# Optimization experiments

Measured on AMD Instinct MI355X. Metric: run time of the kernel, lower is better.

The kernel has to match this reference:

```python
import jax, jax.numpy as jnp
import numpy as np

EPS = 1e-5
NEG_SLOPE = 0.1  # GeoTransformer UnaryBlock uses LeakyReLU(0.1)
GROUPS = 32


def linear(x, W, b):
    # torch nn.Linear convention: W is (out, in)
    return x @ W.T + b


def group_norm(x, gamma, beta, groups=GROUPS):
    # x: (N, C). Torch applies GroupNorm on (1, C, N): stats over (C//g * N) per group.
    N, C = x.shape
    xg = x.T.reshape(groups, -1)            # (g, C//g * N)
    m = xg.mean(axis=1, keepdims=True)
    v = xg.var(axis=1, keepdims=True)
    xn = ((xg - m) / jnp.sqrt(v + EPS)).reshape(C, N).T
    return xn * gamma + beta


def unary_block(x, W, b, gamma, beta):
    return jax.nn.leaky_relu(group_norm(linear(x, W, b), gamma, beta), NEG_SLOPE)


def setup_inputs() -> dict:
    key = jax.random.key(0)
    ks = jax.random.split(key, 24)
    init_dim = 64
    N2, N3, N4, N5 = 131072, 32768, 8192, 2048
    d2, d3, d4, d5 = init_dim * 4, init_dim * 8, init_dim * 16, 2048
    out_dim = 256
    s = lambda k, shp: jax.random.normal(k, shp, dtype=jnp.float32)
    inp = {
        'feats_s2': s(ks[0], (N2, d2)),
        'feats_s3': s(ks[1], (N3, d3)),
        'feats_s4': s(ks[2], (N4, d4)),
        'feats_s5': s(ks[3], (N5, d5)),
        'up1': jax.random.randint(ks[4], (N2,), 0, N3),
        'up2': jax.random.randint(ks[5], (N3,), 0, N4),
        'up3': jax.random.randint(ks[6], (N4,), 0, N5),
        # inproj: Linear(input_dim, init_dim*32)
        'W_in': s(ks[7], (init_dim * 32, d5)) * 0.02,
        'b_in': s(ks[8], (init_dim * 32,)) * 0.02,
        # decoder4: UnaryBlock(init_dim*48, init_dim*16)
        'W4': s(ks[9], (init_dim * 16, init_dim * 48)) * 0.02,
        'b4': s(ks[10], (init_dim * 16,)) * 0.02,
        'g4': jnp.ones((init_dim * 16,), jnp.float32),
        'beta4': jnp.zeros((init_dim * 16,), jnp.float32),
        # decoder3: UnaryBlock(init_dim*24, init_dim*8)
        'W3': s(ks[11], (init_dim * 8, init_dim * 24)) * 0.02,
        'b3': s(ks[12], (init_dim * 8,)) * 0.02,
        'g3': jnp.ones((init_dim * 8,), jnp.float32),
        'beta3': jnp.zeros((init_dim * 8,), jnp.float32),
        # decoder2: LastUnaryBlock(init_dim*12, output_dim) -> plain Linear
        'W2': s(ks[13], (out_dim, init_dim * 12)) * 0.02,
        'b2': s(ks[14], (out_dim,)) * 0.02,
    }
    return inp


def reference(feats_s2, feats_s3, feats_s4, feats_s5, up1, up2, up3,
              W_in, b_in, W4, b4, g4, beta4, W3, b3, g3, beta3, W2, b2):
    x5 = linear(feats_s5, W_in, b_in)                     # (N5, 2048)
    l4 = jnp.concatenate([x5[up3], feats_s4], axis=1)     # gather + concat (N4, 3072)
    l4 = unary_block(l4, W4, b4, g4, beta4)               # (N4, 1024)
    l3 = jnp.concatenate([l4[up2], feats_s3], axis=1)     # (N3, 1536)
    l3 = unary_block(l3, W3, b3, g3, beta3)               # (N3, 512)
    l2 = jnp.concatenate([l3[up1], feats_s2], axis=1)     # (N2, 768)
    return linear(l2, W2, b2)                             # (N2, 256)
```

## Files before the change

kernel.cpp:

```cpp
#include <hip/hip_runtime.h>
#include <cstdint>
#include <cstddef>

#define DEVI __device__ __forceinline__
#define WAITVM0 asm volatile("s_waitcnt vmcnt(0)" ::: "memory")
#define WAITVM4 asm volatile("s_waitcnt vmcnt(4)" ::: "memory")
#define WAITVM8 asm volatile("s_waitcnt vmcnt(8)" ::: "memory")
#define WAITLGKM asm volatile("s_waitcnt lgkmcnt(0)" ::: "memory")
#define SCHEDB __builtin_amdgcn_sched_barrier(0)

typedef __bf16 bf16x8 __attribute__((ext_vector_type(8)));
typedef float f32x4 __attribute__((ext_vector_type(4)));
typedef uint32_t u32x4 __attribute__((ext_vector_type(4)));

DEVI ushort f2bf(float f) {
  union { float f; uint32_t u; } v; v.f = f;
  uint32_t u = v.u;
  return (ushort)((u + 0x7FFFu + ((u >> 16) & 1u)) >> 16);
}
DEVI float bf2f(ushort h) {
  union { uint32_t u; float f; } v; v.u = ((uint32_t)h) << 16;
  return v.f;
}
DEVI float lrelu(float t) { return t > 0.0f ? t : 0.1f * t; }

DEVI u32x4 cvt8(f32x4 a, f32x4 b) {
  u32x4 o;
  o[0] = (uint32_t)f2bf(a[0]) | ((uint32_t)f2bf(a[1]) << 16);
  o[1] = (uint32_t)f2bf(a[2]) | ((uint32_t)f2bf(a[3]) << 16);
  o[2] = (uint32_t)f2bf(b[0]) | ((uint32_t)f2bf(b[1]) << 16);
  o[3] = (uint32_t)f2bf(b[2]) | ((uint32_t)f2bf(b[3]) << 16);
  return o;
}
DEVI u32x4 gn8(u32x4 d, f32x4 g0, f32x4 g1, f32x4 b0, f32x4 b1) {
  float f0 = bf2f((ushort)(d[0] & 0xffffu)), f1 = bf2f((ushort)(d[0] >> 16));
  float f2 = bf2f((ushort)(d[1] & 0xffffu)), f3 = bf2f((ushort)(d[1] >> 16));
  float f4 = bf2f((ushort)(d[2] & 0xffffu)), f5 = bf2f((ushort)(d[2] >> 16));
  float f6 = bf2f((ushort)(d[3] & 0xffffu)), f7 = bf2f((ushort)(d[3] >> 16));
  float t0 = lrelu(f0 * g0[0] + b0[0]), t1 = lrelu(f1 * g0[1] + b0[1]);
  float t2 = lrelu(f2 * g0[2] + b0[2]), t3 = lrelu(f3 * g0[3] + b0[3]);
  float t4 = lrelu(f4 * g1[0] + b1[0]), t5 = lrelu(f5 * g1[1] + b1[1]);
  float t6 = lrelu(f6 * g1[2] + b1[2]), t7 = lrelu(f7 * g1[3] + b1[3]);
  u32x4 o;
  o[0] = (uint32_t)f2bf(t0) | ((uint32_t)f2bf(t1) << 16);
  o[1] = (uint32_t)f2bf(t2) | ((uint32_t)f2bf(t3) << 16);
  o[2] = (uint32_t)f2bf(t4) | ((uint32_t)f2bf(t5) << 16);
  o[3] = (uint32_t)f2bf(t6) | ((uint32_t)f2bf(t7) << 16);
  return o;
}

DEVI void async_copy16(const void* g, void* l) {
  __attribute__((address_space(1))) void* gp =
      reinterpret_cast<__attribute__((address_space(1))) void*>(
          reinterpret_cast<uintptr_t>(const_cast<void*>(g)));
  __attribute__((address_space(3))) void* lp =
      reinterpret_cast<__attribute__((address_space(3))) void*>(
          static_cast<uint32_t>(reinterpret_cast<uintptr_t>(l)));
  __builtin_amdgcn_global_load_lds(gp, lp, 16, 0, 0);
}

struct CvtSeg { const f32x4* src; u32x4* dst; };
struct CvtArgs { CvtSeg seg[4]; int start[5]; };

__global__ void cvt_multi(CvtArgs a, int total8) {
  int i = blockIdx.x * blockDim.x + threadIdx.x;
  const int stride = gridDim.x * blockDim.x;
  for (; i < total8; i += stride) {
    int s = 0;
#pragma unroll
    for (int j = 1; j < 4; ++j) s += (i >= a.start[j]);
    const int off = i - a.start[s];
    f32x4 f0 = a.seg[s].src[off * 2];
    f32x4 f1 = a.seg[s].src[off * 2 + 1];
    a.seg[s].dst[off] = cvt8(f0, f1);
  }
}

__global__ void zero_kernel(float* __restrict__ p) { p[threadIdx.x] = 0.0f; }

__global__ void gn_coef(const float* __restrict__ stats, const float* __restrict__ gamma,
                        const float* __restrict__ beta, float* __restrict__ ga,
                        float* __restrict__ be, int C, float invcnt) {
  int ch = blockIdx.x * blockDim.x + threadIdx.x;
  if (ch >= C) return;
  int g = ch / (C >> 5);
  float mean = stats[2 * g] * invcnt;
  float var = stats[2 * g + 1] * invcnt - mean * mean;
  float inv = rsqrtf(var + 1e-5f);
  float gm = gamma[ch] * inv;
  ga[ch] = gm;
  be[ch] = beta[ch] - mean * gm;
}

__global__ void gn_apply(const ushort* __restrict__ x, const float* __restrict__ ga,
                         const float* __restrict__ be, ushort* __restrict__ y,
                         int Nrows, int C) {
  const int tpr = C >> 3;
  const int gtid = blockIdx.x * blockDim.x + threadIdx.x;
  const int c8 = (gtid % tpr) * 8;
  const f32x4 g0 = *(const f32x4*)(ga + c8), g1 = *(const f32x4*)(ga + c8 + 4);
  const f32x4 b0 = *(const f32x4*)(be + c8), b1 = *(const f32x4*)(be + c8 + 4);
  const int rstep = (gridDim.x * blockDim.x) / tpr;
  for (int r = gtid / tpr; r < Nrows; r += rstep) {
    u32x4 d = *(const u32x4*)(x + (size_t)r * C + c8);
    *(u32x4*)(y + (size_t)r * C + c8) = gn8(d, g0, g1, b0, b1);
  }
}

template <int EPI, int STATS>
__global__ __launch_bounds__(256, 3) void gemms(
    const ushort* __restrict__ Ag, const float* __restrict__ Adf,
    const int* __restrict__ up, int dg,
    const ushort* __restrict__ Bw, const float* __restrict__ bias,
    void* __restrict__ Cout, float* __restrict__ stats,
    int M, int N, int K) {
  constexpr int BM = 128, BN = 128, BK = 64;
  constexpr int ABY = BM * BK * 2;
  __shared__ __align__(16) char smem[ABY + BN * BK * 2];
  __shared__ int s_up[BM];
  __shared__ float ssum[32], ssq[32];

  const int nbn = N >> 7;
  const int cpx = (int)gridDim.x >> 3;
  const int bid = ((int)blockIdx.x & 7) * cpx + ((int)blockIdx.x >> 3);
  const int bm = bid / nbn, bn = bid % nbn;
  const int row0 = bm * BM, col0 = bn * BN;
  const int tid = threadIdx.x, lane = tid & 63, wave = tid >> 6;
  const int wm = wave >> 1, wn = wave & 1;
  const int dd = K - dg;
  const int ng = dg / BK;
  const int nt = K / BK;

  if (up != nullptr && tid < BM) s_up[tid] = up[row0 + tid];
  if constexpr (STATS) { if (tid < 32) { ssum[tid] = 0.f; ssq[tid] = 0.f; } }
  __syncthreads();

  int cs_[4];
  const ushort* pG[4]; const float* pD[4];
#pragma unroll
  for (int li = 0; li < 4; ++li) {
    const int chunk = li * 256 + tid;
    const int r = chunk >> 3;
    cs_[li] = ((chunk & 7) ^ (r & 7)) << 3;
    pG[li] = (ng > 0) ? (Ag + (size_t)s_up[r] * dg + cs_[li]) : nullptr;
    pD[li] = (ng < nt) ? (Adf + (size_t)(row0 + r) * dd + cs_[li]) : nullptr;
  }
  const ushort* pB[4];
#pragma unroll
  for (int li = 0; li < 4; ++li) {
    const int chunk = li * 256 + tid;
    const int rb = chunk >> 3;
    pB[li] = Bw + (size_t)(col0 + rb) * K + (((chunk & 7) ^ (rb & 7)) << 3);
  }

  f32x4 rdv[8];

  auto issueAg = [&](int t) {
#pragma unroll
    for (int li = 0; li < 4; ++li)
      async_copy16(pG[li] + t * BK, smem + li * 4096 + wave * 1024);
  };
  auto issueB = [&](int t) {
#pragma unroll
    for (int li = 0; li < 4; ++li)
      async_copy16(pB[li] + t * BK, smem + ABY + li * 4096 + wave * 1024);
  };
  auto issueRdv = [&](int t) {
    const int kd = t * BK - dg;
#pragma unroll
    for (int li = 0; li < 4; ++li) {
      rdv[2 * li]     = *(const f32x4*)(pD[li] + kd);
      rdv[2 * li + 1] = *(const f32x4*)(pD[li] + kd + 4);
    }
  };
  auto dsWrite = [&]() {
#pragma unroll
    for (int li = 0; li < 4; ++li)
      *(u32x4*)(smem + li * 4096 + tid * 16) = cvt8(rdv[2 * li], rdv[2 * li + 1]);
  };

  int offA[2][4], offB[2][4];
#pragma unroll
  for (int kk = 0; kk < 2; ++kk) {
    const int ch = kk * 4 + (lane >> 4);
#pragma unroll
    for (int m = 0; m < 4; ++m) {
      const int ra = wm * 64 + m * 16 + (lane & 15);
      offA[kk][m] = ra * 128 + ((ch ^ (ra & 7)) << 4);
    }
#pragma unroll
    for (int n = 0; n < 4; ++n) {
      const int rb = wn * 64 + n * 16 + (lane & 15);
      offB[kk][n] = ABY + rb * 128 + ((ch ^ (rb & 7)) << 4);
    }
  }

  if (ng == 0) issueRdv(0);

  f32x4 acc[4][4] = {};
  for (int t = 0; t < nt; ++t) {
    const bool curD = (t >= ng);
    const bool nxtDirect = (t + 1 < nt) && (t + 1 >= ng);
    if (!curD) issueAg(t);
    issueB(t);
    if (curD) {
      WAITVM4;
      SCHEDB;
      dsWrite();
    }
    if (nxtDirect) issueRdv(t + 1);
    if (nxtDirect) { WAITVM8; } else { WAITVM0; }
    WAITLGKM;
    SCHEDB;
    __builtin_amdgcn_s_barrier();
#pragma unroll
    for (int kk = 0; kk < 2; ++kk) {
      bf16x8 af[4], bv[4];
#pragma unroll
      for (int m = 0; m < 4; ++m) af[m] = *(const bf16x8*)(smem + offA[kk][m]);
#pragma unroll
      for (int n = 0; n < 4; ++n) bv[n] = *(const bf16x8*)(smem + offB[kk][n]);
      __builtin_amdgcn_s_setprio(1);
#pragma unroll
      for (int m = 0; m < 4; ++m)
#pragma unroll
        for (int n = 0; n < 4; ++n)
          acc[m][n] = __builtin_amdgcn_mfma_f32_16x16x32_bf16(af[m], bv[n], acc[m][n], 0, 0, 0);
      __builtin_amdgcn_s_setprio(0);
    }
    __builtin_amdgcn_s_barrier();
  }

  const int cr = (lane >> 4) << 2;
  const int cc = lane & 15;
  float sacc[4] = {0, 0, 0, 0}, qacc[4] = {0, 0, 0, 0};
#pragma unroll
  for (int n = 0; n < 4; ++n) {
    const int colg = col0 + wn * 64 + n * 16 + cc;
    const float bvv = bias[colg];
#pragma unroll
    for (int m = 0; m < 4; ++m) {
      const int rowg = row0 + wm * 64 + m * 16 + cr;
#pragma unroll
      for (int r2 = 0; r2 < 4; ++r2) {
        const float v = acc[m][n][r2] + bvv;
        if constexpr (STATS) { sacc[n] += v; qacc[n] += v * v; }
        if constexpr (EPI == 0)
          ((ushort*)Cout)[(size_t)(rowg + r2) * N + colg] = f2bf(v);
        else
          ((float*)Cout)[(size_t)(rowg + r2) * N + colg] = v;
      }
    }
  }
  if constexpr (STATS) {
    const int gsize = N >> 5;
#pragma unroll
    for (int n = 0; n < 4; ++n) {
      float s = sacc[n], q = qacc[n];
      s += __shfl_xor(s, 16); q += __shfl_xor(q, 16);
      s += __shfl_xor(s, 32); q += __shfl_xor(q, 32);
      if (lane < 16) {
        const int colg = col0 + wn * 64 + n * 16 + lane;
        const int g = colg / gsize;
        atomicAdd(&ssum[g], s);
        atomicAdd(&ssq[g], q);
      }
    }
    __syncthreads();
    if (tid < 32) {
      const int g0 = col0 / gsize, g1 = (col0 + BN) / gsize;
      if (tid >= g0 && tid < g1) {
        atomicAdd(&stats[2 * tid], ssum[tid]);
        atomicAdd(&stats[2 * tid + 1], ssq[tid]);
      }
    }
  }
}

template <int EPI, int STATS>
__global__ __launch_bounds__(512, 3) void gemmw(
    const ushort* __restrict__ Ag, const float* __restrict__ Adf,
    const int* __restrict__ up, int dg,
    const ushort* __restrict__ Bw, const float* __restrict__ bias,
    void* __restrict__ Cout, float* __restrict__ stats,
    int M, int N, int K) {
  constexpr int BM = 128, BN = 256, BK = 64;
  constexpr int ABY = BM * BK * 2;
  __shared__ __align__(16) char smem[ABY + BN * BK * 2];
  __shared__ int s_up[BM];
  __shared__ float ssum[32], ssq[32];

  const int nbn = N >> 8;
  const int cpx = (int)gridDim.x >> 3;
  const int bid = ((int)blockIdx.x & 7) * cpx + ((int)blockIdx.x >> 3);
  const int bm = bid / nbn, bn = bid % nbn;
  const int row0 = bm * BM, col0 = bn * BN;
  const int tid = threadIdx.x, lane = tid & 63, wave = tid >> 6;
  const int wm = wave >> 2, wn = wave & 3;
  const int dd = K - dg;
  const int ng = dg / BK;
  const int nt = K / BK;

  if (up != nullptr && tid < BM) s_up[tid] = up[row0 + tid];
  if constexpr (STATS) { if (tid < 32) { ssum[tid] = 0.f; ssq[tid] = 0.f; } }
  __syncthreads();

  int cs_[2];
  const ushort* pG[2]; const float* pD[2];
#pragma unroll
  for (int li = 0; li < 2; ++li) {
    const int chunk = li * 512 + tid;
    const int r = chunk >> 3;
    cs_[li] = ((chunk & 7) ^ (r & 7)) << 3;
    pG[li] = (ng > 0) ? (Ag + (size_t)s_up[r] * dg + cs_[li]) : nullptr;
    pD[li] = (ng < nt) ? (Adf + (size_t)(row0 + r) * dd + cs_[li]) : nullptr;
  }
  const ushort* pB[4];
#pragma unroll
  for (int li = 0; li < 4; ++li) {
    const int chunk = li * 512 + tid;
    const int rb = chunk >> 3;
    pB[li] = Bw + (size_t)(col0 + rb) * K + (((chunk & 7) ^ (rb & 7)) << 3);
  }

  f32x4 rdv[4];

  auto issueAg = [&](int t) {
#pragma unroll
    for (int li = 0; li < 2; ++li)
      async_copy16(pG[li] + t * BK, smem + li * 8192 + wave * 1024);
  };
  auto issueB = [&](int t) {
#pragma unroll
    for (int li = 0; li < 4; ++li)
      async_copy16(pB[li] + t * BK, smem + ABY + li * 8192 + wave * 1024);
  };
  auto issueRdv = [&](int t) {
    const int kd = t * BK - dg;
#pragma unroll
    for (int li = 0; li < 2; ++li) {
      rdv[2 * li]     = *(const f32x4*)(pD[li] + kd);
      rdv[2 * li + 1] = *(const f32x4*)(pD[li] + kd + 4);
    }
  };
  auto dsWrite = [&]() {
#pragma unroll
    for (int li = 0; li < 2; ++li)
      *(u32x4*)(smem + li * 8192 + tid * 16) = cvt8(rdv[2 * li], rdv[2 * li + 1]);
  };

  int offA[2][4], offB[2][4];
#pragma unroll
  for (int kk = 0; kk < 2; ++kk) {
    const int ch = kk * 4 + (lane >> 4);
#pragma unroll
    for (int m = 0; m < 4; ++m) {
      const int ra = wm * 64 + m * 16 + (lane & 15);
      offA[kk][m] = ra * 128 + ((ch ^ (ra & 7)) << 4);
    }
#pragma unroll
    for (int n = 0; n < 4; ++n) {
      const int rb = wn * 64 + n * 16 + (lane & 15);
      offB[kk][n] = ABY + rb * 128 + ((ch ^ (rb & 7)) << 4);
    }
  }

  if (ng == 0) issueRdv(0);

  f32x4 acc[4][4] = {};
  for (int t = 0; t < nt; ++t) {
    const bool curD = (t >= ng);
    const bool nxtD = (t + 1 < nt) && (t + 1 >= ng);
    if (!curD) issueAg(t);
    issueB(t);
    if (curD) {
      WAITVM4;
      SCHEDB;
      dsWrite();
    }
    if (nxtD) issueRdv(t + 1);
    if (nxtD) { WAITVM4; } else { WAITVM0; }
    WAITLGKM;
    SCHEDB;
    __builtin_amdgcn_s_barrier();
#pragma unroll
    for (int kk = 0; kk < 2; ++kk) {
      bf16x8 af[4], bv[4];
#pragma unroll
      for (int m = 0; m < 4; ++m) af[m] = *(const bf16x8*)(smem + offA[kk][m]);
#pragma unroll
      for (int n = 0; n < 4; ++n) bv[n] = *(const bf16x8*)(smem + offB[kk][n]);
      __builtin_amdgcn_s_setprio(1);
#pragma unroll
      for (int m = 0; m < 4; ++m)
#pragma unroll
        for (int n = 0; n < 4; ++n)
          acc[m][n] = __builtin_amdgcn_mfma_f32_16x16x32_bf16(af[m], bv[n], acc[m][n], 0, 0, 0);
      __builtin_amdgcn_s_setprio(0);
    }
    __builtin_amdgcn_s_barrier();
  }

  const int cr = (lane >> 4) << 2;
  const int cc = lane & 15;
  float sacc[4] = {0, 0, 0, 0}, qacc[4] = {0, 0, 0, 0};
#pragma unroll
  for (int n = 0; n < 4; ++n) {
    const int colg = col0 + wn * 64 + n * 16 + cc;
    const float bvv = bias[colg];
#pragma unroll
    for (int m = 0; m < 4; ++m) {
      const int rowg = row0 + wm * 64 + m * 16 + cr;
#pragma unroll
      for (int r2 = 0; r2 < 4; ++r2) {
        const float v = acc[m][n][r2] + bvv;
        if constexpr (STATS) { sacc[n] += v; qacc[n] += v * v; }
        if constexpr (EPI == 0)
          ((ushort*)Cout)[(size_t)(rowg + r2) * N + colg] = f2bf(v);
        else
          ((float*)Cout)[(size_t)(rowg + r2) * N + colg] = v;
      }
    }
  }
  if constexpr (STATS) {
    const int gsize = N >> 5;
#pragma unroll
    for (int n = 0; n < 4; ++n) {
      float s = sacc[n], q = qacc[n];
      s += __shfl_xor(s, 16); q += __shfl_xor(q, 16);
      s += __shfl_xor(s, 32); q += __shfl_xor(q, 32);
      if (lane < 16) {
        const int colg = col0 + wn * 64 + n * 16 + lane;
        const int g = colg / gsize;
        atomicAdd(&ssum[g], s);
        atomicAdd(&ssq[g], q);
      }
    }
    __syncthreads();
    if (tid < 32) {
      const int g0 = col0 / gsize, g1 = (col0 + BN) / gsize;
      if (tid >= g0 && tid < g1) {
        atomicAdd(&stats[2 * tid], ssum[tid]);
        atomicAdd(&stats[2 * tid + 1], ssq[tid]);
      }
    }
  }
}

extern "C" void kernel_launch(void* const* d_in, const int* in_sizes, int n_in,
                              void* d_out, int out_size, void* d_ws, size_t ws_size,
                              hipStream_t stream) {
  const float* s2   = (const float*)d_in[0];
  const float* s3   = (const float*)d_in[1];
  const float* s4   = (const float*)d_in[2];
  const float* s5   = (const float*)d_in[3];
  const int*   up1  = (const int*)d_in[4];
  const int*   up2  = (const int*)d_in[5];
  const int*   up3  = (const int*)d_in[6];
  const float* W_in = (const float*)d_in[7];
  const float* b_in = (const float*)d_in[8];
  const float* W4   = (const float*)d_in[9];
  const float* b4   = (const float*)d_in[10];
  const float* g4   = (const float*)d_in[11];
  const float* bt4  = (const float*)d_in[12];
  const float* W3   = (const float*)d_in[13];
  const float* b3   = (const float*)d_in[14];
  const float* g3   = (const float*)d_in[15];
  const float* bt3  = (const float*)d_in[16];
  const float* W2   = (const float*)d_in[17];
  const float* b2   = (const float*)d_in[18];
  float* out = (float*)d_out;
  char* ws = (char*)d_ws;

  ushort* Winb  = (ushort*)(ws + 0);
  ushort* W4b   = (ushort*)(ws + 8388608);
  ushort* W3b   = (ushort*)(ws + 14680064);
  ushort* W2b   = (ushort*)(ws + 16252928);
  float*  stats = (float*)(ws + 16646144);
  float*  cga4  = (float*)(ws + 16646656);
  float*  cbe4  = (float*)(ws + 16650752);
  float*  cga3  = (float*)(ws + 16654848);
  float*  cbe3  = (float*)(ws + 16656896);
  ushort* x5b   = (ushort*)(ws + 16777216);
  ushort* l4lin = (ushort*)(ws + 25165824);
  ushort* l4b   = (ushort*)(ws + 41943040);
  ushort* l3lin = (ushort*)(ws + 58720256);
  ushort* l3b   = (ushort*)(ws + 92274688);

  zero_kernel<<<1, 128, 0, stream>>>(stats);

  CvtArgs ca;
  const float* srcs[4] = { W_in, W4, W3, W2 };
  ushort* dsts[4] = { Winb, W4b, W3b, W2b };
  long ns[4] = { 2048L*2048, 1024L*3072, 512L*1536, 256L*768 };
  int cum = 0;
  for (int i = 0; i < 4; ++i) {
    ca.seg[i].src = (const f32x4*)srcs[i];
    ca.seg[i].dst = (u32x4*)dsts[i];
    ca.start[i] = cum;
    cum += (int)(ns[i] >> 3);
  }
  ca.start[4] = cum;
  cvt_multi<<<1024, 256, 0, stream>>>(ca, cum);

  gemms<0, 0><<<256, 256, 0, stream>>>(
      nullptr, s5, nullptr, 0, Winb, b_in, x5b, nullptr, 2048, 2048, 2048);
  gemmw<0, 1><<<256, 512, 0, stream>>>(
      x5b, s4, up3, 2048, W4b, b4, l4lin, stats, 8192, 1024, 3072);
  gn_coef<<<4, 256, 0, stream>>>(stats, g4, bt4, cga4, cbe4, 1024, 1.0f / 262144.0f);
  gn_apply<<<2048, 256, 0, stream>>>(l4lin, cga4, cbe4, l4b, 8192, 1024);
  gemmw<0, 1><<<512, 512, 0, stream>>>(
      l4b, s3, up2, 1024, W3b, b3, l3lin, stats + 64, 32768, 512, 1536);
  gn_coef<<<2, 256, 0, stream>>>(stats + 64, g3, bt3, cga3, cbe3, 512, 1.0f / 524288.0f);
  gn_apply<<<2048, 256, 0, stream>>>(l3lin, cga3, cbe3, l3b, 32768, 512);
  gemmw<1, 0><<<1024, 512, 0, stream>>>(
      l3b, s2, up1, 512, W2b, b2, out, nullptr, 131072, 256, 768);

  (void)in_sizes; (void)n_in; (void)out_size; (void)ws_size;
}
```

Before: 362.5 us.

## Fuse GroupNorm into decoder GEMMs via cooperative grid sync

Replaces the GEMM → gn_coef → gn_apply sequence for decoder4 and decoder3 with one cooperative kernel. Each block keeps its accumulators in registers, adds its group statistics atomically, waits on a grid-wide sync, then applies the normalisation and LeakyReLU before writing bf16 output. This removes the intermediate pre-norm write and re-read plus two launches per layer. In exchange it uses 128x128 tiles with 256 threads, needs SUB=2 row tiles held in registers for layer 3, and depends on all 512 blocks being co-resident. The final linear layer also moves from the wide kernel to the 128x128 kernel.

```diff
diff --git a/kernel.cpp b/kernel.cpp
--- a/kernel.cpp
+++ b/kernel.cpp
@@ -1,4 +1,5 @@
 #include <hip/hip_runtime.h>
+#include <hip/hip_cooperative_groups.h>
 #include <cstdint>
 #include <cstddef>
 
@@ -30,22 +31,6 @@
   o[1] = (uint32_t)f2bf(a[2]) | ((uint32_t)f2bf(a[3]) << 16);
   o[2] = (uint32_t)f2bf(b[0]) | ((uint32_t)f2bf(b[1]) << 16);
   o[3] = (uint32_t)f2bf(b[2]) | ((uint32_t)f2bf(b[3]) << 16);
-  return o;
-}
-DEVI u32x4 gn8(u32x4 d, f32x4 g0, f32x4 g1, f32x4 b0, f32x4 b1) {
-  float f0 = bf2f((ushort)(d[0] & 0xffffu)), f1 = bf2f((ushort)(d[0] >> 16));
-  float f2 = bf2f((ushort)(d[1] & 0xffffu)), f3 = bf2f((ushort)(d[1] >> 16));
-  float f4 = bf2f((ushort)(d[2] & 0xffffu)), f5 = bf2f((ushort)(d[2] >> 16));
-  float f6 = bf2f((ushort)(d[3] & 0xffffu)), f7 = bf2f((ushort)(d[3] >> 16));
-  float t0 = lrelu(f0 * g0[0] + b0[0]), t1 = lrelu(f1 * g0[1] + b0[1]);
-  float t2 = lrelu(f2 * g0[2] + b0[2]), t3 = lrelu(f3 * g0[3] + b0[3]);
-  float t4 = lrelu(f4 * g1[0] + b1[0]), t5 = lrelu(f5 * g1[1] + b1[1]);
-  float t6 = lrelu(f6 * g1[2] + b1[2]), t7 = lrelu(f7 * g1[3] + b1[3]);
-  u32x4 o;
-  o[0] = (uint32_t)f2bf(t0) | ((uint32_t)f2bf(t1) << 16);
-  o[1] = (uint32_t)f2bf(t2) | ((uint32_t)f2bf(t3) << 16);
-  o[2] = (uint32_t)f2bf(t4) | ((uint32_t)f2bf(t5) << 16);
-  o[3] = (uint32_t)f2bf(t6) | ((uint32_t)f2bf(t7) << 16);
   return o;
 }
 
@@ -77,35 +62,6 @@
 }
 
 __global__ void zero_kernel(float* __restrict__ p) { p[threadIdx.x] = 0.0f; }
-
-__global__ void gn_coef(const float* __restrict__ stats, const float* __restrict__ gamma,
-                        const float* __restrict__ beta, float* __restrict__ ga,
-                        float* __restrict__ be, int C, float invcnt) {
-  int ch = blockIdx.x * blockDim.x + threadIdx.x;
-  if (ch >= C) return;
-  int g = ch / (C >> 5);
-  float mean = stats[2 * g] * invcnt;
-  float var = stats[2 * g + 1] * invcnt - mean * mean;
-  float inv = rsqrtf(var + 1e-5f);
-  float gm = gamma[ch] * inv;
-  ga[ch] = gm;
-  be[ch] = beta[ch] - mean * gm;
-}
-
-__global__ void gn_apply(const ushort* __restrict__ x, const float* __restrict__ ga,
-                         const float* __restrict__ be, ushort* __restrict__ y,
-                         int Nrows, int C) {
-  const int tpr = C >> 3;
-  const int gtid = blockIdx.x * blockDim.x + threadIdx.x;
-  const int c8 = (gtid % tpr) * 8;
-  const f32x4 g0 = *(const f32x4*)(ga + c8), g1 = *(const f32x4*)(ga + c8 + 4);
-  const f32x4 b0 = *(const f32x4*)(be + c8), b1 = *(const f32x4*)(be + c8 + 4);
-  const int rstep = (gridDim.x * blockDim.x) / tpr;
-  for (int r = gtid / tpr; r < Nrows; r += rstep) {
-    u32x4 d = *(const u32x4*)(x + (size_t)r * C + c8);
-    *(u32x4*)(y + (size_t)r * C + c8) = gn8(d, g0, g1, b0, b1);
-  }
-}
 
 template <int EPI, int STATS>
 __global__ __launch_bounds__(256, 3) void gemms(
@@ -277,77 +233,42 @@
   }
 }
 
-template <int EPI, int STATS>
-__global__ __launch_bounds__(512, 3) void gemmw(
+template <int SUB>
+__global__ void gemmc(
     const ushort* __restrict__ Ag, const float* __restrict__ Adf,
     const int* __restrict__ up, int dg,
     const ushort* __restrict__ Bw, const float* __restrict__ bias,
-    void* __restrict__ Cout, float* __restrict__ stats,
-    int M, int N, int K) {
-  constexpr int BM = 128, BN = 256, BK = 64;
+    const float* __restrict__ gamma, const float* __restrict__ beta,
+    ushort* __restrict__ Cout, float* __restrict__ stats,
+    int M, int N, int K, float invcnt) {
+  constexpr int BM = 128, BN = 128, BK = 64;
   constexpr int ABY = BM * BK * 2;
   __shared__ __align__(16) char smem[ABY + BN * BK * 2];
   __shared__ int s_up[BM];
   __shared__ float ssum[32], ssq[32];
-
-  const int nbn = N >> 8;
+  __shared__ float sst[64];
+
+  const int nbn = N >> 7;
   const int cpx = (int)gridDim.x >> 3;
   const int bid = ((int)blockIdx.x & 7) * cpx + ((int)blockIdx.x >> 3);
-  const int bm = bid / nbn, bn = bid % nbn;
-  const int row0 = bm * BM, col0 = bn * BN;
+  const int bm0 = (bid / nbn) * SUB;
+  const int bn = bid % nbn;
+  const int col0 = bn * BN;
   const int tid = threadIdx.x, lane = tid & 63, wave = tid >> 6;
-  const int wm = wave >> 2, wn = wave & 3;
+  const int wm = wave >> 1, wn = wave & 1;
   const int dd = K - dg;
   const int ng = dg / BK;
   const int nt = K / BK;
 
-  if (up != nullptr && tid < BM) s_up[tid] = up[row0 + tid];
-  if constexpr (STATS) { if (tid < 32) { ssum[tid] = 0.f; ssq[tid] = 0.f; } }
-  __syncthreads();
-
-  int cs_[2];
-  const ushort* pG[2]; const float* pD[2];
-#pragma unroll
-  for (int li = 0; li < 2; ++li) {
-    const int chunk = li * 512 + tid;
-    const int r = chunk >> 3;
-    cs_[li] = ((chunk & 7) ^ (r & 7)) << 3;
-    pG[li] = (ng > 0) ? (Ag + (size_t)s_up[r] * dg + cs_[li]) : nullptr;
-    pD[li] = (ng < nt) ? (Adf + (size_t)(row0 + r) * dd + cs_[li]) : nullptr;
-  }
+  if (tid < 32) { ssum[tid] = 0.f; ssq[tid] = 0.f; }
+
   const ushort* pB[4];
 #pragma unroll
   for (int li = 0; li < 4; ++li) {
-    const int chunk = li * 512 + tid;
+    const int chunk = li * 256 + tid;
     const int rb = chunk >> 3;
     pB[li] = Bw + (size_t)(col0 + rb) * K + (((chunk & 7) ^ (rb & 7)) << 3);
   }
-
-  f32x4 rdv[4];
-
-  auto issueAg = [&](int t) {
-#pragma unroll
-    for (int li = 0; li < 2; ++li)
-      async_copy16(pG[li] + t * BK, smem + li * 8192 + wave * 1024);
-  };
-  auto issueB = [&](int t) {
-#pragma unroll
-    for (int li = 0; li < 4; ++li)
-      async_copy16(pB[li] + t * BK, smem + ABY + li * 8192 + wave * 1024);
-  };
-  auto issueRdv = [&](int t) {
-    const int kd = t * BK - dg;
-#pragma unroll
-    for (int li = 0; li < 2; ++li) {
-      rdv[2 * li]     = *(const f32x4*)(pD[li] + kd);
-      rdv[2 * li + 1] = *(const f32x4*)(pD[li] + kd + 4);
-    }
-  };
-  auto dsWrite = [&]() {
-#pragma unroll
-    for (int li = 0; li < 2; ++li)
-      *(u32x4*)(smem + li * 8192 + tid * 16) = cvt8(rdv[2 * li], rdv[2 * li + 1]);
-  };
 
   int offA[2][4], offB[2][4];
 #pragma unroll
@@ -365,83 +286,152 @@
     }
   }
 
-  if (ng == 0) issueRdv(0);
-
-  f32x4 acc[4][4] = {};
-  for (int t = 0; t < nt; ++t) {
-    const bool curD = (t >= ng);
-    const bool nxtD = (t + 1 < nt) && (t + 1 >= ng);
-    if (!curD) issueAg(t);
-    issueB(t);
-    if (curD) {
-      WAITVM4;
+  f32x4 acc[SUB][4][4] = {};
+
+#pragma unroll
+  for (int s = 0; s < SUB; ++s) {
+    const int row0 = (bm0 + s) * BM;
+    __syncthreads();
+    if (tid < BM) s_up[tid] = up[row0 + tid];
+    __syncthreads();
+
+    int cs_[4];
+    const ushort* pG[4]; const float* pD[4];
+#pragma unroll
+    for (int li = 0; li < 4; ++li) {
+      const int chunk = li * 256 + tid;
+      const int r = chunk >> 3;
+      cs_[li] = ((chunk & 7) ^ (r & 7)) << 3;
+      pG[li] = Ag + (size_t)s_up[r] * dg + cs_[li];
+      pD[li] = Adf + (size_t)(row0 + r) * dd + cs_[li];
+    }
+
+    f32x4 rdv[8];
+    auto issueAg = [&](int t) {
+#pragma unroll
+      for (int li = 0; li < 4; ++li)
+        async_copy16(pG[li] + t * BK, smem + li * 4096 + wave * 1024);
+    };
+    auto issueB = [&](int t) {
+#pragma unroll
+      for (int li = 0; li < 4; ++li)
+        async_copy16(pB[li] + t * BK, smem + ABY + li * 4096 + wave * 1024);
+    };
+    auto issueRdv = [&](int t) {
+      const int kd = t * BK - dg;
+#pragma unroll
+      for (int li = 0; li < 4; ++li) {
+        rdv[2 * li]     = *(const f32x4*)(pD[li] + kd);
+        rdv[2 * li + 1] = *(const f32x4*)(pD[li] + kd + 4);
+      }
+    };
+    auto dsWrite = [&]() {
+#pragma unroll
+      for (int li = 0; li < 4; ++li)
+        *(u32x4*)(smem + li * 4096 + tid * 16) = cvt8(rdv[2 * li], rdv[2 * li + 1]);
+    };
+
+    if (ng == 0) issueRdv(0);
+
+    for (int t = 0; t < nt; ++t) {
+      const bool curD = (t >= ng);
+      const bool nxtDirect = (t + 1 < nt) && (t + 1 >= ng);
+      if (!curD) issueAg(t);
+      issueB(t);
+      if (curD) {
+        WAITVM4;
+        SCHEDB;
+        dsWrite();
+      }
+      if (nxtDirect) issueRdv(t + 1);
+      if (nxtDirect) { WAITVM8; } else { WAITVM0; }
+      WAITLGKM;
       SCHEDB;
-      dsWrite();
-    }
-    if (nxtD) issueRdv(t + 1);
-    if (nxtD) { WAITVM4; } else { WAITVM0; }
-    WAITLGKM;
-    SCHEDB;
-    __builtin_amdgcn_s_barrier();
-#pragma unroll
-    for (int kk = 0; kk < 2; ++kk) {
-      bf16x8 af[4], bv[4];
-#pragma unroll
-      for (int m = 0; m < 4; ++m) af[m] = *(const bf16x8*)(smem + offA[kk][m]);
-#pragma unroll
-      for (int n = 0; n < 4; ++n) bv[n] = *(const bf16x8*)(smem + offB[kk][n]);
-      __builtin_amdgcn_s_setprio(1);
-#pragma unroll
-      for (int m = 0; m < 4; ++m)
-#pragma unroll
-        for (int n = 0; n < 4; ++n)
-          acc[m][n] = __builtin_amdgcn_mfma_f32_16x16x32_bf16(af[m], bv[n], acc[m][n], 0, 0, 0);
-      __builtin_amdgcn_s_setprio(0);
-    }
-    __builtin_amdgcn_s_barrier();
+      __builtin_amdgcn_s_barrier();
+#pragma unroll
+      for (int kk = 0; kk < 2; ++kk) {
+        bf16x8 af[4], bv[4];
+#pragma unroll
+        for (int m = 0; m < 4; ++m) af[m] = *(const bf16x8*)(smem + offA[kk][m]);
+#pragma unroll
+        for (int n = 0; n < 4; ++n) bv[n] = *(const bf16x8*)(smem + offB[kk][n]);
+        __builtin_amdgcn_s_setprio(1);
+#pragma unroll
+        for (int m = 0; m < 4; ++m)
+#pragma unroll
+          for (int n = 0; n < 4; ++n)
+            acc[s][m][n] = __builtin_amdgcn_mfma_f32_16x16x32_bf16(af[m], bv[n], acc[s][m][n], 0, 0, 0);
+        __builtin_amdgcn_s_setprio(0);
+      }
+      __builtin_amdgcn_s_barrier();
+    }
   }
 
   const int cr = (lane >> 4) << 2;
   const int cc = lane & 15;
+  const int gsize = N >> 5;
   float sacc[4] = {0, 0, 0, 0}, qacc[4] = {0, 0, 0, 0};
 #pragma unroll
   for (int n = 0; n < 4; ++n) {
     const int colg = col0 + wn * 64 + n * 16 + cc;
     const float bvv = bias[colg];
 #pragma unroll
-    for (int m = 0; m < 4; ++m) {
-      const int rowg = row0 + wm * 64 + m * 16 + cr;
-#pragma unroll
-      for (int r2 = 0; r2 < 4; ++r2) {
-        const float v = acc[m][n][r2] + bvv;
-        if constexpr (STATS) { sacc[n] += v; qacc[n] += v * v; }
-        if constexpr (EPI == 0)
-          ((ushort*)Cout)[(size_t)(rowg + r2) * N + colg] = f2bf(v);
-        else
-          ((float*)Cout)[(size_t)(rowg + r2) * N + colg] = v;
-      }
-    }
-  }
-  if constexpr (STATS) {
-    const int gsize = N >> 5;
-#pragma unroll
-    for (int n = 0; n < 4; ++n) {
-      float s = sacc[n], q = qacc[n];
-      s += __shfl_xor(s, 16); q += __shfl_xor(q, 16);
-      s += __shfl_xor(s, 32); q += __shfl_xor(q, 32);
-      if (lane < 16) {
-        const int colg = col0 + wn * 64 + n * 16 + lane;
-        const int g = colg / gsize;
-        atomicAdd(&ssum[g], s);
-        atomicAdd(&ssq[g], q);
-      }
-    }
-    __syncthreads();
-    if (tid < 32) {
-      const int g0 = col0 / gsize, g1 = (col0 + BN) / gsize;
-      if (tid >= g0 && tid < g1) {
-        atomicAdd(&stats[2 * tid], ssum[tid]);
-        atomicAdd(&stats[2 * tid + 1], ssq[tid]);
+    for (int s = 0; s < SUB; ++s)
+#pragma unroll
+      for (int m = 0; m < 4; ++m)
+#pragma unroll
+        for (int r2 = 0; r2 < 4; ++r2) {
+          const float v = acc[s][m][n][r2] + bvv;
+          sacc[n] += v; qacc[n] += v * v;
+        }
+  }
+#pragma unroll
+  for (int n = 0; n < 4; ++n) {
+    float s = sacc[n], q = qacc[n];
+    s += __shfl_xor(s, 16); q += __shfl_xor(q, 16);
+    s += __shfl_xor(s, 32); q += __shfl_xor(q, 32);
+    if (lane < 16) {
+      const int colg = col0 + wn * 64 + n * 16 + lane;
+      const int g = colg / gsize;
+      atomicAdd(&ssum[g], s);
+      atomicAdd(&ssq[g], q);
+    }
+  }
+  __syncthreads();
+  if (tid < 32) {
+    const int g0 = col0 / gsize, g1 = (col0 + BN) / gsize;
+    if (tid >= g0 && tid < g1) {
+      atomicAdd(&stats[2 * tid], ssum[tid]);
+      atomicAdd(&stats[2 * tid + 1], ssq[tid]);
+    }
+  }
+
+  cooperative_groups::this_grid().sync();
+
+  if (tid < 64) sst[tid] = atomicAdd(&stats[tid], 0.0f);
+  __syncthreads();
+
+#pragma unroll
+  for (int n = 0; n < 4; ++n) {
+    const int colg = col0 + wn * 64 + n * 16 + cc;
+    const int g = colg / gsize;
+    const float mean = sst[2 * g] * invcnt;
+    const float var  = sst[2 * g + 1] * invcnt - mean * mean;
+    const float inv  = rsqrtf(var + 1e-5f);
+    const float ga = gamma[colg] * inv;
+    const float be = beta[colg] - mean * ga;
+    const float bvv = bias[colg];
+#pragma unroll
+    for (int s = 0; s < SUB; ++s) {
+      const int row0 = (bm0 + s) * BM;
+#pragma unroll
+      for (int m = 0; m < 4; ++m) {
+        const int rowg = row0 + wm * 64 + m * 16 + cr;
+#pragma unroll
+        for (int r2 = 0; r2 < 4; ++r2) {
+          const float v = acc[s][m][n][r2] + bvv;
+          Cout[(size_t)(rowg + r2) * N + colg] = f2bf(lrelu(v * ga + be));
+        }
       }
     }
   }
@@ -477,15 +467,9 @@
   ushort* W3b   = (ushort*)(ws + 14680064);
   ushort* W2b   = (ushort*)(ws + 16252928);
   float*  stats = (float*)(ws + 16646144);
-  float*  cga4  = (float*)(ws + 16646656);
-  float*  cbe4  = (float*)(ws + 16650752);
-  float*  cga3  = (float*)(ws + 16654848);
-  float*  cbe3  = (float*)(ws + 16656896);
   ushort* x5b   = (ushort*)(ws + 16777216);
-  ushort* l4lin = (ushort*)(ws + 25165824);
-  ushort* l4b   = (ushort*)(ws + 41943040);
-  ushort* l3lin = (ushort*)(ws + 58720256);
-  ushort* l3b   = (ushort*)(ws + 92274688);
+  ushort* l4b   = (ushort*)(ws + 25165824);
+  ushort* l3b   = (ushort*)(ws + 41943040);
 
   zero_kernel<<<1, 128, 0, stream>>>(stats);
 
@@ -505,15 +489,26 @@
 
   gemms<0, 0><<<256, 256, 0, stream>>>(
       nullptr, s5, nullptr, 0, Winb, b_in, x5b, nullptr, 2048, 2048, 2048);
-  gemmw<0, 1><<<256, 512, 0, stream>>>(
-      x5b, s4, up3, 2048, W4b, b4, l4lin, stats, 8192, 1024, 3072);
-  gn_coef<<<4, 256, 0, stream>>>(stats, g4, bt4, cga4, cbe4, 1024, 1.0f / 262144.0f);
-  gn_apply<<<2048, 256, 0, stream>>>(l4lin, cga4, cbe4, l4b, 8192, 1024);
-  gemmw<0, 1><<<512, 512, 0, stream>>>(
-      l4b, s3, up2, 1024, W3b, b3, l3lin, stats + 64, 32768, 512, 1536);
-  gn_coef<<<2, 256, 0, stream>>>(stats + 64, g3, bt3, cga3, cbe3, 512, 1.0f / 524288.0f);
-  gn_apply<<<2048, 256, 0, stream>>>(l3lin, cga3, cbe3, l3b, 32768, 512);
-  gemmw<1, 0><<<1024, 512, 0, stream>>>(
+
+  {
+    const ushort* a = x5b; const float* ad = s4; const int* u = up3; int dgv = 2048;
+    const ushort* b = W4b; const float* bi = b4; const float* ga = g4; const float* be = bt4;
+    ushort* co = l4b; float* st = stats;
+    int Mv = 8192, Nv = 1024, Kv = 3072; float ic = 1.0f / 262144.0f;
+    void* args[] = { &a, &ad, &u, &dgv, &b, &bi, &ga, &be, &co, &st, &Mv, &Nv, &Kv, &ic };
+    hipLaunchCooperativeKernel(gemmc<1>, dim3(512), dim3(256), args, 0, stream);
+  }
+
+  {
+    const ushort* a = l4b; const float* ad = s3; const int* u = up2; int dgv = 1024;
+    const ushort* b = W3b; const float* bi = b3; const float* ga = g3; const float* be = bt3;
+    ushort* co = l3b; float* st = stats + 64;
+    int Mv = 32768, Nv = 512, Kv = 1536; float ic = 1.0f / 524288.0f;
+    void* args[] = { &a, &ad, &u, &dgv, &b, &bi, &ga, &be, &co, &st, &Mv, &Nv, &Kv, &ic };
+    hipLaunchCooperativeKernel(gemmc<2>, dim3(512), dim3(256), args, 0, stream);
+  }
+
+  gemms<1, 0><<<2048, 256, 0, stream>>>(
       l3b, s2, up1, 512, W2b, b2, out, nullptr, 131072, 256, 768);
 
   (void)in_sizes; (void)n_in; (void)out_size; (void)ws_size;
```

Measured after the change: 867.9 us. 139% more time.
